# Kernel optimization log

Hardware: AMD Instinct MI355X
Metric: run time of the kernel (lower is better)

Reference implementation:

```python
import jax, jax.numpy as jnp
import numpy as np

B, N, C = 8, 2048, 1024
SPARSITY = 0.8
K_KEEP = int(N * SPARSITY)  # 1638
NEG = 1e10


def setup_inputs() -> dict:
    key = jax.random.key(0)
    ks = jax.random.split(key, 7)
    s = 1.0 / np.sqrt(C)
    return {
        "x": jax.random.normal(ks[0], (B, N, C), dtype=jnp.float32),
        "Wq": jax.random.uniform(ks[1], (C, C), dtype=jnp.float32, minval=-s, maxval=s),
        "bq": jax.random.uniform(ks[2], (C,), dtype=jnp.float32, minval=-s, maxval=s),
        "Wk": jax.random.uniform(ks[3], (C, C), dtype=jnp.float32, minval=-s, maxval=s),
        "bk": jax.random.uniform(ks[4], (C,), dtype=jnp.float32, minval=-s, maxval=s),
        "Wv": jax.random.uniform(ks[5], (C, C), dtype=jnp.float32, minval=-s, maxval=s),
        "bv": jax.random.uniform(ks[6], (C,), dtype=jnp.float32, minval=-s, maxval=s),
    }


def reference(x, Wq, bq, Wk, bk, Wv, bv):
    # Linear projections (torch Linear: y = x @ W.T + b)
    Q = jnp.einsum("bnc,dc->bnd", x, Wq) + bq
    Kt = jnp.einsum("bnc,dc->bnd", x, Wk) + bk
    V = jnp.einsum("bnc,dc->bnd", x, Wv) + bv
    attn = jnp.einsum("bnd,bmd->bnm", Q, Kt) / jnp.sqrt(jnp.float32(C))  # [B,N,N]
    _, idx = jax.lax.top_k(attn, K_KEEP)  # idx: [B,N,K_KEEP]
    bI = jnp.arange(B)[:, None, None]
    nI = jnp.arange(N)[None, :, None]
    mask = jnp.zeros_like(attn).at[bI, nI, idx].set(1.0)
    attn = attn * mask - NEG * (1.0 - mask)
    attn = jax.nn.softmax(attn, axis=-1)
    return jnp.einsum("bnm,bmd->bnd", attn, V)
```

## Files before the change

kernel.cpp:

```cpp
#include <hip/hip_runtime.h>

typedef _Float16 f16;
typedef __attribute__((ext_vector_type(8))) _Float16 f16x8;
typedef __attribute__((ext_vector_type(4))) _Float16 f16x4;
typedef __attribute__((ext_vector_type(4))) float f32x4;

constexpr int BB = 8;
constexpr int NN = 2048;
constexpr int CC = 1024;
constexpr int MTOT = BB * NN;
constexpr int KKEEP = 1638;

__device__ __forceinline__ void gl_lds16(const void* g, void* l) {
  __builtin_amdgcn_global_load_lds((__attribute__((address_space(1))) void*)g,
                                   (__attribute__((address_space(3))) void*)l,
                                   16, 0, 0);
}

__global__ __launch_bounds__(256) void cvt_f32_f16(const float* __restrict__ s,
                                                   f16* __restrict__ d, int n4) {
  int i = blockIdx.x * 256 + threadIdx.x;
  if (i < n4) {
    float4 f = ((const float4*)s)[i];
    f16x4 o = {(f16)f.x, (f16)f.y, (f16)f.z, (f16)f.w};
    ((f16x4*)d)[i] = o;
  }
}

template <int MODE>
__global__ __launch_bounds__(256, 2) void gemm_bt(
    const f16* __restrict__ A, const f16* __restrict__ B,
    const float* __restrict__ bias, void* __restrict__ Cout,
    int K, int lda, int ldb, int ldc, float scale, int ldct,
    long strideA, long strideB, long strideC) {
  const f16* Ab = A + (size_t)blockIdx.z * strideA;
  const f16* Bbp = B + (size_t)blockIdx.z * strideB;

  const int bm = blockIdx.x * 128;
  const int bn = blockIdx.y * 128;
  const int tid = threadIdx.x;
  const int wave = tid >> 6;
  const int lane = tid & 63;
  const int wy = wave >> 1, wx = wave & 1;

  __shared__ f16 As[128 * 32];
  __shared__ f16 Bs[128 * 32];

  f32x4 acc[4][4];
#pragma unroll
  for (int i = 0; i < 4; i++)
#pragma unroll
    for (int j = 0; j < 4; j++) acc[i][j] = (f32x4){0.f, 0.f, 0.f, 0.f};

  const int sr = wave * 32 + (lane >> 2);
  const int sc = (lane & 3) * 8;
  const f16* gA0 = Ab + (size_t)(bm + sr) * lda + sc;
  const f16* gA1 = gA0 + (size_t)16 * lda;
  const f16* gB0 = Bbp + (size_t)(bn + sr) * ldb + sc;
  const f16* gB1 = gB0 + (size_t)16 * ldb;
  f16* lA0 = As + (wave * 32) * 32;
  f16* lA1 = As + (wave * 32 + 16) * 32;
  f16* lB0 = Bs + (wave * 32) * 32;
  f16* lB1 = Bs + (wave * 32 + 16) * 32;

  const int frm = wy * 64 + (lane & 15);
  const int frn = wx * 64 + (lane & 15);
  const int kq = (lane >> 4) * 8;

  for (int k0 = 0; k0 < K; k0 += 32) {
    gl_lds16(gA0 + k0, lA0);
    gl_lds16(gA1 + k0, lA1);
    gl_lds16(gB0 + k0, lB0);
    gl_lds16(gB1 + k0, lB1);
    __syncthreads();
    f16x8 av[4], bv[4];
#pragma unroll
    for (int i = 0; i < 4; i++)
      av[i] = *(const f16x8*)(As + (frm + 16 * i) * 32 + kq);
#pragma unroll
    for (int i = 0; i < 4; i++)
      bv[i] = *(const f16x8*)(Bs + (frn + 16 * i) * 32 + kq);
#pragma unroll
    for (int i = 0; i < 4; i++)
#pragma unroll
      for (int j = 0; j < 4; j++)
        acc[i][j] =
            __builtin_amdgcn_mfma_f32_16x16x32_f16(av[i], bv[j], acc[i][j], 0, 0, 0);
    __syncthreads();
  }

  const int q = lane >> 4;
  const int ci = lane & 15;
#pragma unroll
  for (int i = 0; i < 4; i++) {
#pragma unroll
    for (int j = 0; j < 4; j++) {
      const int row0 = bm + wy * 64 + i * 16 + q * 4;
      const int col = bn + wx * 64 + j * 16 + ci;
      if (MODE == 0) {
        float* C = (float*)Cout + (size_t)blockIdx.z * strideC;
#pragma unroll
        for (int r = 0; r < 4; r++)
          C[(size_t)(row0 + r) * ldc + col] = acc[i][j][r] * scale;
      } else if (MODE == 1) {
        f16* C = (f16*)Cout + (size_t)blockIdx.z * strideC;
        const float bb = bias[col];
#pragma unroll
        for (int r = 0; r < 4; r++)
          C[(size_t)(row0 + r) * ldc + col] = (f16)(acc[i][j][r] + bb);
      } else {
        f16* C = (f16*)Cout;
        const float bb = bias[col];
        f16x4 o;
#pragma unroll
        for (int r = 0; r < 4; r++) o[r] = (f16)(acc[i][j][r] + bb);
        *(f16x4*)(C + (size_t)col * ldct + row0) = o;
      }
    }
  }
}

__global__ __launch_bounds__(256) void topk_softmax_kernel(float* __restrict__ S) {
  const size_t row = blockIdx.x;
  float* srow = S + row * 2048;
  f16* prow = (f16*)srow;
  const int t = threadIdx.x;

  float v[8];
  float4 f0 = ((const float4*)srow)[2 * t];
  float4 f1 = ((const float4*)srow)[2 * t + 1];
  v[0] = f0.x; v[1] = f0.y; v[2] = f0.z; v[3] = f0.w;
  v[4] = f1.x; v[5] = f1.y; v[6] = f1.z; v[7] = f1.w;

  unsigned u[8];
#pragma unroll
  for (int j = 0; j < 8; j++) {
    unsigned b = __float_as_uint(v[j]);
    u[j] = (b & 0x80000000u) ? ~b : (b | 0x80000000u);
  }

  __shared__ int hist[256];
  __shared__ int sA[256], sB[256];
  __shared__ unsigned sh_thr;
  __shared__ int sh_want;
  __shared__ float sh_f[256];

  unsigned prefix = 0;
  int want = KKEEP;
  for (int shift = 24; shift >= 0; shift -= 8) {
    hist[t] = 0;
    __syncthreads();
#pragma unroll
    for (int j = 0; j < 8; j++) {
      bool cand = (shift == 24) || ((u[j] >> (shift + 8)) == (prefix >> (shift + 8)));
      if (cand) atomicAdd(&hist[(u[j] >> shift) & 255], 1);
    }
    __syncthreads();
    {
      int* src = sA;
      int* dst = sB;
      src[t] = hist[t];
      __syncthreads();
      for (int off = 1; off < 256; off <<= 1) {
        int x = src[t] + ((t + off < 256) ? src[t + off] : 0);
        dst[t] = x;
        __syncthreads();
        int* tmp = src; src = dst; dst = tmp;
      }
      int cum = src[t];
      int above = (t < 255) ? src[t + 1] : 0;
      if (cum >= want && above < want) {
        sh_thr = prefix | ((unsigned)t << shift);
        sh_want = want - above;
      }
    }
    __syncthreads();
    prefix = sh_thr;
    want = sh_want;
    __syncthreads();
  }

  int eqf[8];
  int ceq = 0;
#pragma unroll
  for (int j = 0; j < 8; j++) {
    eqf[j] = (u[j] == prefix) ? 1 : 0;
    ceq += eqf[j];
  }
  int excl;
  {
    int* src = sA;
    int* dst = sB;
    src[t] = ceq;
    __syncthreads();
    for (int off = 1; off < 256; off <<= 1) {
      int x = src[t] + ((t >= off) ? src[t - off] : 0);
      dst[t] = x;
      __syncthreads();
      int* tmp = src; src = dst; dst = tmp;
    }
    excl = src[t] - ceq;
    __syncthreads();
  }

  float mx = v[0];
#pragma unroll
  for (int j = 1; j < 8; j++) mx = fmaxf(mx, v[j]);
  sh_f[t] = mx;
  __syncthreads();
  for (int s = 128; s > 0; s >>= 1) {
    if (t < s) sh_f[t] = fmaxf(sh_f[t], sh_f[t + s]);
    __syncthreads();
  }
  mx = sh_f[0];
  __syncthreads();

  float e[8];
  float lsum = 0.f;
  int r = excl;
#pragma unroll
  for (int j = 0; j < 8; j++) {
    bool kept;
    if (u[j] > prefix) {
      kept = true;
    } else if (eqf[j]) {
      kept = (r < want);
      r++;
    } else {
      kept = false;
    }
    e[j] = kept ? expf(v[j] - mx) : 0.f;
    lsum += e[j];
  }
  sh_f[t] = lsum;
  __syncthreads();
  for (int s = 128; s > 0; s >>= 1) {
    if (t < s) sh_f[t] += sh_f[t + s];
    __syncthreads();
  }
  const float inv = 1.0f / sh_f[0];

  f16x8 o;
#pragma unroll
  for (int j = 0; j < 8; j++) o[j] = (f16)(e[j] * inv);
  *(f16x8*)(prow + t * 8) = o;
}

extern "C" void kernel_launch(void* const* d_in, const int* in_sizes, int n_in,
                              void* d_out, int out_size, void* d_ws, size_t ws_size,
                              hipStream_t stream) {
  (void)in_sizes; (void)n_in; (void)out_size; (void)ws_size;
  const float* x = (const float*)d_in[0];
  const float* Wq = (const float*)d_in[1];
  const float* bq = (const float*)d_in[2];
  const float* Wk = (const float*)d_in[3];
  const float* bk = (const float*)d_in[4];
  const float* Wv = (const float*)d_in[5];
  const float* bv = (const float*)d_in[6];
  float* out = (float*)d_out;

  char* ws = (char*)d_ws;
  f16* qb = (f16*)(ws + 0);
  f16* kb = (f16*)(ws + 33554432);
  f16* vtb = (f16*)(ws + 67108864);
  float* S = (float*)(ws + 100663296);
  f16* xb = (f16*)(ws + 100663296);
  f16* wqb = (f16*)(ws + 134217728);
  f16* wkb = (f16*)(ws + 136314880);
  f16* wvb = (f16*)(ws + 138412032);

  cvt_f32_f16<<<(MTOT * CC / 4 + 255) / 256, 256, 0, stream>>>(x, xb, MTOT * CC / 4);
  cvt_f32_f16<<<(CC * CC / 4 + 255) / 256, 256, 0, stream>>>(Wq, wqb, CC * CC / 4);
  cvt_f32_f16<<<(CC * CC / 4 + 255) / 256, 256, 0, stream>>>(Wk, wkb, CC * CC / 4);
  cvt_f32_f16<<<(CC * CC / 4 + 255) / 256, 256, 0, stream>>>(Wv, wvb, CC * CC / 4);

  gemm_bt<1><<<dim3(MTOT / 128, CC / 128, 1), 256, 0, stream>>>(
      xb, wqb, bq, qb, CC, CC, CC, CC, 1.f, 0, 0, 0, 0);
  gemm_bt<1><<<dim3(MTOT / 128, CC / 128, 1), 256, 0, stream>>>(
      xb, wkb, bk, kb, CC, CC, CC, CC, 1.f, 0, 0, 0, 0);
  gemm_bt<2><<<dim3(MTOT / 128, CC / 128, 1), 256, 0, stream>>>(
      xb, wvb, bv, vtb, CC, CC, CC, 0, 1.f, MTOT, 0, 0, 0);

  gemm_bt<0><<<dim3(NN / 128, NN / 128, BB), 256, 0, stream>>>(
      qb, kb, nullptr, S, CC, CC, CC, NN, 1.f / 32.f, 0,
      (long)NN * CC, (long)NN * CC, (long)NN * NN);

  topk_softmax_kernel<<<MTOT, 256, 0, stream>>>(S);

  gemm_bt<0><<<dim3(NN / 128, CC / 128, BB), 256, 0, stream>>>(
      (const f16*)S, vtb, nullptr, out, NN, 2 * NN, MTOT, CC, 1.f, 0,
      (long)NN * 2 * NN, (long)NN, (long)NN * CC);
}
```

Baseline: 536.4 us.

## Use wave-shuffle scans and per-wave histograms in top-k softmax kernel

Replaces the shared-memory Hillis-Steele scans and tree reductions in the radix-select top-k softmax with 64-lane shuffle scans/reductions plus a small cross-wave aggregate, removing most block barriers. Splits the radix histogram into per-wave copies to reduce LDS atomic contention. Switches expf to __expf for cheaper exponentials at slightly lower accuracy.

```diff
diff --git a/kernel.cpp b/kernel.cpp
--- a/kernel.cpp
+++ b/kernel.cpp
@@ -125,6 +125,8 @@
   float* srow = S + row * 2048;
   f16* prow = (f16*)srow;
   const int t = threadIdx.x;
+  const int lane = t & 63;
+  const int wave = t >> 6;
 
   float v[8];
   float4 f0 = ((const float4*)srow)[2 * t];
@@ -139,45 +141,45 @@
     u[j] = (b & 0x80000000u) ? ~b : (b | 0x80000000u);
   }
 
-  __shared__ int hist[256];
-  __shared__ int sA[256], sB[256];
+  __shared__ int hist4[256 * 4];
+  __shared__ int wagg[4];
+  __shared__ float wf[4];
   __shared__ unsigned sh_thr;
   __shared__ int sh_want;
-  __shared__ float sh_f[256];
 
   unsigned prefix = 0;
   int want = KKEEP;
   for (int shift = 24; shift >= 0; shift -= 8) {
-    hist[t] = 0;
+    ((int4*)hist4)[t] = (int4){0, 0, 0, 0};
     __syncthreads();
 #pragma unroll
     for (int j = 0; j < 8; j++) {
       bool cand = (shift == 24) || ((u[j] >> (shift + 8)) == (prefix >> (shift + 8)));
-      if (cand) atomicAdd(&hist[(u[j] >> shift) & 255], 1);
-    }
-    __syncthreads();
-    {
-      int* src = sA;
-      int* dst = sB;
-      src[t] = hist[t];
-      __syncthreads();
-      for (int off = 1; off < 256; off <<= 1) {
-        int x = src[t] + ((t + off < 256) ? src[t + off] : 0);
-        dst[t] = x;
-        __syncthreads();
-        int* tmp = src; src = dst; dst = tmp;
-      }
-      int cum = src[t];
-      int above = (t < 255) ? src[t + 1] : 0;
-      if (cum >= want && above < want) {
-        sh_thr = prefix | ((unsigned)t << shift);
-        sh_want = want - above;
-      }
+      if (cand) atomicAdd(&hist4[(((u[j] >> shift) & 255) << 2) + wave], 1);
+    }
+    __syncthreads();
+    int4 hh = ((const int4*)hist4)[t];
+    int h = hh.x + hh.y + hh.z + hh.w;
+    int sfx = h;
+#pragma unroll
+    for (int off = 1; off < 64; off <<= 1) {
+      int o = __shfl_down(sfx, off, 64);
+      sfx += (lane + off < 64) ? o : 0;
+    }
+    if (lane == 0) wagg[wave] = sfx;
+    __syncthreads();
+    int hi = 0;
+#pragma unroll
+    for (int w = 0; w < 4; w++) hi += (w > wave) ? wagg[w] : 0;
+    const int cum = sfx + hi;
+    const int above = cum - h;
+    if (cum >= want && above < want) {
+      sh_thr = prefix | ((unsigned)t << shift);
+      sh_want = want - above;
     }
     __syncthreads();
     prefix = sh_thr;
     want = sh_want;
-    __syncthreads();
   }
 
   int eqf[8];
@@ -187,32 +189,27 @@
     eqf[j] = (u[j] == prefix) ? 1 : 0;
     ceq += eqf[j];
   }
-  int excl;
-  {
-    int* src = sA;
-    int* dst = sB;
-    src[t] = ceq;
-    __syncthreads();
-    for (int off = 1; off < 256; off <<= 1) {
-      int x = src[t] + ((t >= off) ? src[t - off] : 0);
-      dst[t] = x;
-      __syncthreads();
-      int* tmp = src; src = dst; dst = tmp;
-    }
-    excl = src[t] - ceq;
-    __syncthreads();
-  }
+  int inc = ceq;
+#pragma unroll
+  for (int off = 1; off < 64; off <<= 1) {
+    int o = __shfl_up(inc, off, 64);
+    inc += (lane >= off) ? o : 0;
+  }
+  if (lane == 63) wagg[wave] = inc;
+  __syncthreads();
+  int pre = 0;
+#pragma unroll
+  for (int w = 0; w < 4; w++) pre += (w < wave) ? wagg[w] : 0;
+  const int excl = pre + inc - ceq;
 
   float mx = v[0];
 #pragma unroll
   for (int j = 1; j < 8; j++) mx = fmaxf(mx, v[j]);
-  sh_f[t] = mx;
-  __syncthreads();
-  for (int s = 128; s > 0; s >>= 1) {
-    if (t < s) sh_f[t] = fmaxf(sh_f[t], sh_f[t + s]);
-    __syncthreads();
-  }
-  mx = sh_f[0];
+#pragma unroll
+  for (int off = 32; off > 0; off >>= 1) mx = fmaxf(mx, __shfl_xor(mx, off, 64));
+  if (lane == 0) wf[wave] = mx;
+  __syncthreads();
+  mx = fmaxf(fmaxf(wf[0], wf[1]), fmaxf(wf[2], wf[3]));
   __syncthreads();
 
   float e[8];
@@ -229,16 +226,14 @@
     } else {
       kept = false;
     }
-    e[j] = kept ? expf(v[j] - mx) : 0.f;
+    e[j] = kept ? __expf(v[j] - mx) : 0.f;
     lsum += e[j];
   }
-  sh_f[t] = lsum;
-  __syncthreads();
-  for (int s = 128; s > 0; s >>= 1) {
-    if (t < s) sh_f[t] += sh_f[t + s];
-    __syncthreads();
-  }
-  const float inv = 1.0f / sh_f[0];
+#pragma unroll
+  for (int off = 32; off > 0; off >>= 1) lsum += __shfl_xor(lsum, off, 64);
+  if (lane == 0) wf[wave] = lsum;
+  __syncthreads();
+  const float inv = 1.0f / (wf[0] + wf[1] + wf[2] + wf[3]);
 
   f16x8 o;
 #pragma unroll
```

Measured after the change: 534.9 us. Within noise of the previous version (-0.3%).
